# Kernel optimization log

Measured on AMD Instinct MI355X. Metric: run time of the kernel, lower is better.

Reference implementation:

```python
import jax, jax.numpy as jnp
import numpy as np

EPS = 1e-12          # sinkhorn_knopp epsilon
LOW, HIGH = 0.02, 0.98  # SquashedSigmoid bounds
N_ITERS = 10         # num_iterations
BATCH = 2097152


def setup_inputs() -> dict:
    key = jax.random.key(0)
    ks = jax.random.split(key, 9)
    dims = [6, 64, 32, 16, 9]
    inp = {"margins": jax.random.uniform(ks[0], (BATCH, 6), jnp.float32, 0.05, 1.0)}
    for i in range(4):
        fi, fo = dims[i], dims[i + 1]
        inp[f"W{i+1}"] = jax.random.normal(ks[1 + 2 * i], (fi, fo), jnp.float32) / np.float32(np.sqrt(fi))
        inp[f"b{i+1}"] = jnp.zeros((fo,), jnp.float32)
    return inp


def _mlp(x, W1, b1, W2, b2, W3, b3, W4, b4):
    h = jax.nn.relu(x @ W1 + b1)
    h = jax.nn.relu(h @ W2 + b2)
    h = jax.nn.relu(h @ W3 + b3)
    return h @ W4 + b4  # [B, 9]


def _tau(p4):
    # user-supplied tau: 4 positive params -> 3x3 matrix; 2x2 block padded with ones
    B = p4.shape[0]
    A = jnp.ones((B, 3, 3), p4.dtype)
    return A.at[:, :2, :2].set(p4.reshape(B, 2, 2))


def _sinkhorn_knopp(A, r, c):
    # batched row/col balancing; per-sample A is 3x3, r/c are length-3 margins
    for _ in range(N_ITERS):
        A = A * (r[:, :, None] / (A.sum(axis=2, keepdims=True) + EPS))
        A = A * (c[:, None, :] / (A.sum(axis=1, keepdims=True) + EPS))
    return A


def reference(margins, W1, b1, W2, b2, W3, b3, W4, b4):
    B = margins.shape[0]
    M, F = margins[:, 0:3], margins[:, 3:6]
    pars = _mlp(margins, W1, b1, W2, b2, W3, b3, W4, b4)
    muc = _tau(jnp.exp(pars[:, 0:4]))                     # [B,3,3]
    sqs = lambda x: LOW + (HIGH - LOW) * jax.nn.sigmoid(x)
    shm, shf = sqs(pars[:, 4:6]), sqs(pars[:, 6:8])
    V = jnp.exp(pars[:, -1])                              # [B]
    ones = jnp.ones((B, 1), margins.dtype)
    shm0 = jnp.concatenate([shm, ones], axis=1)           # [B,3]
    shf0 = jnp.concatenate([shf, ones], axis=1)
    mucm0, muc0f = M * shm0, F * shf0                     # row / col margins
    mum0, mu0f = M * (1 - shm0), F * (1 - shf0)
    muc = _sinkhorn_knopp(muc, mucm0, muc0f)              # [B,3,3]
    top = jnp.concatenate([muc, mum0[:, :, None]], axis=2)                    # [B,3,4]
    bot = jnp.concatenate([mu0f[:, None, :], jnp.zeros((B, 1, 1), margins.dtype)], axis=2)  # [B,1,4]
    mus = jnp.concatenate([top, bot], axis=1)             # [B,4,4]
    return (mus, V)
```

## Files before the change

kernel.cpp:

```cpp
#include <hip/hip_runtime.h>

typedef _Float16 f16x8 __attribute__((ext_vector_type(8)));
typedef _Float16 f16x4 __attribute__((ext_vector_type(4)));
typedef float    f32x4 __attribute__((ext_vector_type(4)));

static constexpr float kLOW  = 0.02f;
static constexpr float kHIGH = 0.98f;

__device__ __forceinline__ float fast_sigmoid(float v) {
    return 1.0f / (1.0f + __expf(-v));
}
__device__ __forceinline__ float fast_rcp(float v) {
    return __builtin_amdgcn_rcpf(v);
}

__global__ __launch_bounds__(256, 4) void sinkhorn_mlp_mfma(
    const float* __restrict__ margins,
    const float* __restrict__ W1, const float* __restrict__ b1,
    const float* __restrict__ W2, const float* __restrict__ b2,
    const float* __restrict__ W3, const float* __restrict__ b3,
    const float* __restrict__ W4, const float* __restrict__ b4,
    float* __restrict__ out_mus, float* __restrict__ out_V, int B)
{
    __shared__ __align__(16) char smem_all[4 * 9216];
    const int lane = threadIdx.x & 63;
    const int wid  = threadIdx.x >> 6;
    char* smem = smem_all + wid * 9216;

    const int n16 = lane & 15;
    const int q   = lane >> 4;

    const int row  = blockIdx.x * 256 + wid * 64 + lane;
    const int rowC = row < B ? row : (B - 1);

    float x[6];
    {
        const float* mp = margins + (size_t)rowC * 6;
#pragma unroll
        for (int i = 0; i < 6; ++i) x[i] = mp[i];
    }

    {
        f16x8 xr;
#pragma unroll
        for (int j = 0; j < 8; ++j) xr[j] = (_Float16)0.0f;
#pragma unroll
        for (int i = 0; i < 6; ++i) xr[i] = (_Float16)x[i];
        *(f16x8*)(smem + 8176 + lane * 16) = xr;
        if (lane == 0) {
            f16x8 z;
#pragma unroll
            for (int j = 0; j < 8; ++j) z[j] = (_Float16)0.0f;
            *(f16x8*)(smem + 9200) = z;
        }
    }

    f16x8 A1[4];
#pragma unroll
    for (int mt = 0; mt < 4; ++mt)
#pragma unroll
        for (int j = 0; j < 8; ++j) A1[mt][j] = (_Float16)0.0f;
    if (q == 0) {
#pragma unroll
        for (int mt = 0; mt < 4; ++mt)
#pragma unroll
            for (int j = 0; j < 6; ++j)
                A1[mt][j] = (_Float16)W1[j * 64 + mt * 16 + n16];
    }

    f16x8 A2w[2][2];
#pragma unroll
    for (int mt = 0; mt < 2; ++mt)
#pragma unroll
        for (int kt = 0; kt < 2; ++kt)
#pragma unroll
            for (int j = 0; j < 8; ++j)
                A2w[mt][kt][j] = (_Float16)W2[(kt*32 + q*8 + j)*32 + mt*16 + n16];

    f16x8 A3w;
#pragma unroll
    for (int j = 0; j < 8; ++j)
        A3w[j] = (_Float16)W3[(q*8 + j)*16 + n16];

    f32x4 b1v[4], b2v[2], b3v;
#pragma unroll
    for (int mt = 0; mt < 4; ++mt) b1v[mt] = *(const f32x4*)(b1 + mt*16 + q*4);
#pragma unroll
    for (int mt = 0; mt < 2; ++mt) b2v[mt] = *(const f32x4*)(b2 + mt*16 + q*4);
    b3v = *(const f32x4*)(b3 + q*4);

    f16x8 BX[4];
    {
        const int xo   = (q == 0) ? (8176 + n16 * 16) : 9200;
        const int step = (q == 0) ? 256 : 0;
#pragma unroll
        for (int nt = 0; nt < 4; ++nt)
            BX[nt] = *(const f16x8*)(smem + xo + nt * step);
    }
#pragma unroll
    for (int mt = 0; mt < 4; ++mt) {
#pragma unroll
        for (int nt = 0; nt < 4; ++nt) {
            f32x4 C = b1v[mt];
            C = __builtin_amdgcn_mfma_f32_16x16x32_f16(A1[mt], BX[nt], C, 0, 0, 0);
            f16x4 hv;
#pragma unroll
            for (int r = 0; r < 4; ++r) hv[r] = (_Float16)fmaxf(C[r], 0.0f);
            *(f16x4*)(smem + (nt*16 + n16) * 144 + mt*32 + q*8) = hv;
        }
    }

    f16x8 H1f[4][2];
#pragma unroll
    for (int nt = 0; nt < 4; ++nt)
#pragma unroll
        for (int kt = 0; kt < 2; ++kt)
            H1f[nt][kt] = *(const f16x8*)(smem + (nt*16 + n16) * 144 + kt*64 + q*16);
#pragma unroll
    for (int mt = 0; mt < 2; ++mt) {
#pragma unroll
        for (int nt = 0; nt < 4; ++nt) {
            f32x4 C = b2v[mt];
            C = __builtin_amdgcn_mfma_f32_16x16x32_f16(A2w[mt][0], H1f[nt][0], C, 0, 0, 0);
            C = __builtin_amdgcn_mfma_f32_16x16x32_f16(A2w[mt][1], H1f[nt][1], C, 0, 0, 0);
            f16x4 hv;
#pragma unroll
            for (int r = 0; r < 4; ++r) hv[r] = (_Float16)fmaxf(C[r], 0.0f);
            *(f16x4*)(smem + (nt*16 + n16) * 80 + mt*32 + q*8) = hv;
        }
    }

    f16x8 H2f[4];
#pragma unroll
    for (int nt = 0; nt < 4; ++nt)
        H2f[nt] = *(const f16x8*)(smem + (nt*16 + n16) * 80 + q*16);
#pragma unroll
    for (int nt = 0; nt < 4; ++nt) {
        f32x4 C = b3v;
        C = __builtin_amdgcn_mfma_f32_16x16x32_f16(A3w, H2f[nt], C, 0, 0, 0);
        f32x4 o;
#pragma unroll
        for (int r = 0; r < 4; ++r) o[r] = fmaxf(C[r], 0.0f);
        *(f32x4*)(smem + (nt*16 + n16) * 80 + q*16) = o;
    }

    float h3[16];
    {
        const char* rp = smem + lane * 80;
#pragma unroll
        for (int i = 0; i < 4; ++i)
            *(f32x4*)&h3[4*i] = *(const f32x4*)(rp + i * 16);
    }

    float p[9];
#pragma unroll
    for (int k = 0; k < 9; ++k) p[k] = fmaf(h3[0], W4[k], b4[k]);
#pragma unroll
    for (int j = 1; j < 16; ++j) {
        const float hj = h3[j];
        const float* w = W4 + j * 9;
#pragma unroll
        for (int k = 0; k < 9; ++k) p[k] = fmaf(hj, w[k], p[k]);
    }

    const float K00 = __expf(p[0]), K01 = __expf(p[1]);
    const float K10 = __expf(p[2]), K11 = __expf(p[3]);

    const float sh_m0 = kLOW + (kHIGH - kLOW) * fast_sigmoid(p[4]);
    const float sh_m1 = kLOW + (kHIGH - kLOW) * fast_sigmoid(p[5]);
    const float sh_f0 = kLOW + (kHIGH - kLOW) * fast_sigmoid(p[6]);
    const float sh_f1 = kLOW + (kHIGH - kLOW) * fast_sigmoid(p[7]);
    const float V = __expf(p[8]);

    const float M0 = x[0], M1 = x[1], M2 = x[2];
    const float F0 = x[3], F1 = x[4], F2 = x[5];

    const float r0 = M0 * sh_m0, r1 = M1 * sh_m1, r2 = M2;
    const float c0 = F0 * sh_f0, c1 = F1 * sh_f1, c2 = F2;
    const float mum0_0 = M0 * (1.0f - sh_m0), mum0_1 = M1 * (1.0f - sh_m1);
    const float mu0f_0 = F0 * (1.0f - sh_f0), mu0f_1 = F1 * (1.0f - sh_f1);

    const float rc2 = fast_rcp(c2);
    const float g0 = c0 * rc2, g1 = c1 * rc2;
    float v0 = 1.0f, v1 = 1.0f;
    float u0, u1, u2;
#pragma unroll
    for (int it = 0; it < 9; ++it) {
        const float s0 = fmaf(K00, v0, fmaf(K01, v1, 1.0f));
        const float s1 = fmaf(K10, v0, fmaf(K11, v1, 1.0f));
        const float s2 = v0 + v1 + 1.0f;
        u0 = r0 * fast_rcp(s0);
        u1 = r1 * fast_rcp(s1);
        u2 = r2 * fast_rcp(s2);
        const float t0 = fmaf(K00, u0, fmaf(K10, u1, u2));
        const float t1 = fmaf(K01, u0, fmaf(K11, u1, u2));
        const float t2 = u0 + u1 + u2;
        v0 = g0 * (t2 * fast_rcp(t0));
        v1 = g1 * (t2 * fast_rcp(t1));
    }
    float vf0, vf1, vf2;
    {
        const float s0 = fmaf(K00, v0, fmaf(K01, v1, 1.0f));
        const float s1 = fmaf(K10, v0, fmaf(K11, v1, 1.0f));
        const float s2 = v0 + v1 + 1.0f;
        u0 = r0 * fast_rcp(s0);
        u1 = r1 * fast_rcp(s1);
        u2 = r2 * fast_rcp(s2);
        const float t0 = fmaf(K00, u0, fmaf(K10, u1, u2));
        const float t1 = fmaf(K01, u0, fmaf(K11, u1, u2));
        const float t2 = u0 + u1 + u2;
        vf0 = c0 * fast_rcp(t0);
        vf1 = c1 * fast_rcp(t1);
        vf2 = c2 * fast_rcp(t2);
    }
    const float A00 = u0 * K00 * vf0, A01 = u0 * K01 * vf1, A02 = u0 * vf2;
    const float A10 = u1 * K10 * vf0, A11 = u1 * K11 * vf1, A12 = u1 * vf2;
    const float A20 = u2 * vf0,       A21 = u2 * vf1,       A22 = u2 * vf2;

    if (row < B) {
        float4* o = (float4*)(out_mus + (size_t)row * 16);
        o[0] = make_float4(A00, A01, A02, mum0_0);
        o[1] = make_float4(A10, A11, A12, mum0_1);
        o[2] = make_float4(A20, A21, A22, 0.0f);
        o[3] = make_float4(mu0f_0, mu0f_1, 0.0f, 0.0f);
        out_V[row] = V;
    }
}

extern "C" void kernel_launch(void* const* d_in, const int* in_sizes, int n_in,
                              void* d_out, int out_size, void* d_ws, size_t ws_size,
                              hipStream_t stream) {
    const float* margins = (const float*)d_in[0];
    const float* W1 = (const float*)d_in[1];
    const float* b1 = (const float*)d_in[2];
    const float* W2 = (const float*)d_in[3];
    const float* b2 = (const float*)d_in[4];
    const float* W3 = (const float*)d_in[5];
    const float* b3 = (const float*)d_in[6];
    const float* W4 = (const float*)d_in[7];
    const float* b4 = (const float*)d_in[8];

    const int B = in_sizes[0] / 6;
    float* out_mus = (float*)d_out;
    float* out_V   = out_mus + (size_t)B * 16;

    dim3 block(256);
    dim3 grid((B + 255) / 256);
    hipLaunchKernelGGL(sinkhorn_mlp_mfma, grid, block, 0, stream,
                       margins, W1, b1, W2, b2, W3, b3, W4, b4,
                       out_mus, out_V, B);
}
```

Before: 227.1 us.

## Precompute MFMA weight fragments in prep kernel and run last layer on MFMA

A one-block prep kernel converts the weights and biases into per-lane fp16 MFMA fragment layout in the workspace, so each main-kernel wave loads ready fragments with vector loads instead of strided scalar loads and fp32-to-fp16 conversions. The final 16-to-9 layer now runs as an MFMA with an fp16 layer-3 activation, replacing 144 scalar FMAs per row. Margins are read as float2 and the sigmoid uses the hardware reciprocal. This adds a second launch and lowers the last layer to fp16 inputs, which may affect accuracy.

Result: no change. 224.5 us (-1.2%).

```diff
diff --git a/kernel.cpp b/kernel.cpp
--- a/kernel.cpp
+++ b/kernel.cpp
@@ -7,19 +7,94 @@
 static constexpr float kLOW  = 0.02f;
 static constexpr float kHIGH = 0.98f;
 
-__device__ __forceinline__ float fast_sigmoid(float v) {
-    return 1.0f / (1.0f + __expf(-v));
-}
 __device__ __forceinline__ float fast_rcp(float v) {
     return __builtin_amdgcn_rcpf(v);
 }
-
-__global__ __launch_bounds__(256, 4) void sinkhorn_mlp_mfma(
-    const float* __restrict__ margins,
+__device__ __forceinline__ float fast_sigmoid(float v) {
+    return fast_rcp(1.0f + __expf(-v));
+}
+
+enum : int {
+    WS_A1 = 0,
+    WS_A2 = 4096,
+    WS_A3 = 8192,
+    WS_A4 = 9216,
+    WS_B1 = 10240,
+    WS_B2 = 14336,
+    WS_B3 = 16384,
+    WS_B4 = 17408,
+    WS_TOTAL = 18432
+};
+
+__global__ __launch_bounds__(256) void prep_frags(
     const float* __restrict__ W1, const float* __restrict__ b1,
     const float* __restrict__ W2, const float* __restrict__ b2,
     const float* __restrict__ W3, const float* __restrict__ b3,
     const float* __restrict__ W4, const float* __restrict__ b4,
+    char* __restrict__ ws)
+{
+    const int lane = threadIdx.x & 63;
+    const int wid  = threadIdx.x >> 6;
+    const int n16  = lane & 15;
+    const int q    = lane >> 4;
+
+    if (wid == 0) {
+#pragma unroll
+        for (int mt = 0; mt < 4; ++mt) {
+            f16x8 a;
+#pragma unroll
+            for (int j = 0; j < 8; ++j) a[j] = (_Float16)0.0f;
+            if (q == 0) {
+#pragma unroll
+                for (int j = 0; j < 6; ++j)
+                    a[j] = (_Float16)W1[j * 64 + mt * 16 + n16];
+            }
+            ((f16x8*)(ws + WS_A1))[mt * 64 + lane] = a;
+        }
+#pragma unroll
+        for (int mt = 0; mt < 4; ++mt)
+            ((f32x4*)(ws + WS_B1))[mt * 64 + lane] = *(const f32x4*)(b1 + mt * 16 + q * 4);
+    } else if (wid == 1) {
+#pragma unroll
+        for (int mt = 0; mt < 2; ++mt)
+#pragma unroll
+            for (int kt = 0; kt < 2; ++kt) {
+                f16x8 a;
+#pragma unroll
+                for (int j = 0; j < 8; ++j)
+                    a[j] = (_Float16)W2[(kt * 32 + q * 8 + j) * 32 + mt * 16 + n16];
+                ((f16x8*)(ws + WS_A2))[(mt * 2 + kt) * 64 + lane] = a;
+            }
+    } else if (wid == 2) {
+        f16x8 a3;
+#pragma unroll
+        for (int j = 0; j < 8; ++j)
+            a3[j] = (_Float16)W3[(q * 8 + j) * 16 + n16];
+        ((f16x8*)(ws + WS_A3))[lane] = a3;
+        f16x8 a4;
+#pragma unroll
+        for (int j = 0; j < 8; ++j) {
+            const int k = q * 8 + j;
+            a4[j] = (k < 16 && n16 < 9) ? (_Float16)W4[k * 9 + n16] : (_Float16)0.0f;
+        }
+        ((f16x8*)(ws + WS_A4))[lane] = a4;
+    } else {
+#pragma unroll
+        for (int mt = 0; mt < 2; ++mt)
+            ((f32x4*)(ws + WS_B2))[mt * 64 + lane] = *(const f32x4*)(b2 + mt * 16 + q * 4);
+        ((f32x4*)(ws + WS_B3))[lane] = *(const f32x4*)(b3 + q * 4);
+        f32x4 bb;
+#pragma unroll
+        for (int r = 0; r < 4; ++r) {
+            const int m = q * 4 + r;
+            bb[r] = (m < 9) ? b4[m] : 0.0f;
+        }
+        ((f32x4*)(ws + WS_B4))[lane] = bb;
+    }
+}
+
+__global__ __launch_bounds__(256, 4) void sinkhorn_mlp_mfma(
+    const float* __restrict__ margins, const char* __restrict__ ws,
     float* __restrict__ out_mus, float* __restrict__ out_V, int B)
 {
     __shared__ __align__(16) char smem_all[4 * 9216];
@@ -35,9 +110,9 @@
 
     float x[6];
     {
-        const float* mp = margins + (size_t)rowC * 6;
-#pragma unroll
-        for (int i = 0; i < 6; ++i) x[i] = mp[i];
+        const float2* mp = (const float2*)(margins + (size_t)rowC * 6);
+        const float2 a = mp[0], b = mp[1], c = mp[2];
+        x[0] = a.x; x[1] = a.y; x[2] = b.x; x[3] = b.y; x[4] = c.x; x[5] = c.y;
     }
 
     {
@@ -55,39 +130,24 @@
         }
     }
 
-    f16x8 A1[4];
-#pragma unroll
-    for (int mt = 0; mt < 4; ++mt)
-#pragma unroll
-        for (int j = 0; j < 8; ++j) A1[mt][j] = (_Float16)0.0f;
-    if (q == 0) {
-#pragma unroll
-        for (int mt = 0; mt < 4; ++mt)
-#pragma unroll
-            for (int j = 0; j < 6; ++j)
-                A1[mt][j] = (_Float16)W1[j * 64 + mt * 16 + n16];
-    }
-
-    f16x8 A2w[2][2];
+    f16x8 A1[4], A2w[2][2], A3w, A4w;
+#pragma unroll
+    for (int mt = 0; mt < 4; ++mt) A1[mt] = ((const f16x8*)(ws + WS_A1))[mt * 64 + lane];
 #pragma unroll
     for (int mt = 0; mt < 2; ++mt)
 #pragma unroll
         for (int kt = 0; kt < 2; ++kt)
-#pragma unroll
-            for (int j = 0; j < 8; ++j)
-                A2w[mt][kt][j] = (_Float16)W2[(kt*32 + q*8 + j)*32 + mt*16 + n16];
-
-    f16x8 A3w;
-#pragma unroll
-    for (int j = 0; j < 8; ++j)
-        A3w[j] = (_Float16)W3[(q*8 + j)*16 + n16];
-
-    f32x4 b1v[4], b2v[2], b3v;
-#pragma unroll
-    for (int mt = 0; mt < 4; ++mt) b1v[mt] = *(const f32x4*)(b1 + mt*16 + q*4);
-#pragma unroll
-    for (int mt = 0; mt < 2; ++mt) b2v[mt] = *(const f32x4*)(b2 + mt*16 + q*4);
-    b3v = *(const f32x4*)(b3 + q*4);
+            A2w[mt][kt] = ((const f16x8*)(ws + WS_A2))[(mt * 2 + kt) * 64 + lane];
+    A3w = ((const f16x8*)(ws + WS_A3))[lane];
+    A4w = ((const f16x8*)(ws + WS_A4))[lane];
+
+    f32x4 b1v[4], b2v[2], b3v, b4v;
+#pragma unroll
+    for (int mt = 0; mt < 4; ++mt) b1v[mt] = ((const f32x4*)(ws + WS_B1))[mt * 64 + lane];
+#pragma unroll
+    for (int mt = 0; mt < 2; ++mt) b2v[mt] = ((const f32x4*)(ws + WS_B2))[mt * 64 + lane];
+    b3v = ((const f32x4*)(ws + WS_B3))[lane];
+    b4v = ((const f32x4*)(ws + WS_B4))[lane];
 
     f16x8 BX[4];
     {
@@ -138,29 +198,31 @@
     for (int nt = 0; nt < 4; ++nt) {
         f32x4 C = b3v;
         C = __builtin_amdgcn_mfma_f32_16x16x32_f16(A3w, H2f[nt], C, 0, 0, 0);
-        f32x4 o;
-#pragma unroll
-        for (int r = 0; r < 4; ++r) o[r] = fmaxf(C[r], 0.0f);
-        *(f32x4*)(smem + (nt*16 + n16) * 80 + q*16) = o;
-    }
-
-    float h3[16];
-    {
-        const char* rp = smem + lane * 80;
-#pragma unroll
-        for (int i = 0; i < 4; ++i)
-            *(f32x4*)&h3[4*i] = *(const f32x4*)(rp + i * 16);
+        f16x4 hv;
+#pragma unroll
+        for (int r = 0; r < 4; ++r) hv[r] = (_Float16)fmaxf(C[r], 0.0f);
+        *(f16x4*)(smem + (nt*16 + n16) * 32 + q*8) = hv;
+    }
+
+    f16x8 B4[4];
+#pragma unroll
+    for (int nt = 0; nt < 4; ++nt) {
+        const int off = (q < 2) ? ((nt*16 + n16) * 32 + q * 16) : 9200;
+        B4[nt] = *(const f16x8*)(smem + off);
+    }
+#pragma unroll
+    for (int nt = 0; nt < 4; ++nt) {
+        f32x4 C = b4v;
+        C = __builtin_amdgcn_mfma_f32_16x16x32_f16(A4w, B4[nt], C, 0, 0, 0);
+        *(f32x4*)(smem + 2560 + (nt*16 + n16) * 80 + q * 16) = C;
     }
 
     float p[9];
-#pragma unroll
-    for (int k = 0; k < 9; ++k) p[k] = fmaf(h3[0], W4[k], b4[k]);
-#pragma unroll
-    for (int j = 1; j < 16; ++j) {
-        const float hj = h3[j];
-        const float* w = W4 + j * 9;
-#pragma unroll
-        for (int k = 0; k < 9; ++k) p[k] = fmaf(hj, w[k], p[k]);
+    {
+        const char* pr = smem + 2560 + lane * 80;
+        *(f32x4*)&p[0] = *(const f32x4*)(pr);
+        *(f32x4*)&p[4] = *(const f32x4*)(pr + 16);
+        p[8] = *(const float*)(pr + 32);
     }
 
     const float K00 = __expf(p[0]), K01 = __expf(p[1]);
@@ -243,10 +305,13 @@
     const int B = in_sizes[0] / 6;
     float* out_mus = (float*)d_out;
     float* out_V   = out_mus + (size_t)B * 16;
+    char*  ws      = (char*)d_ws;
+
+    hipLaunchKernelGGL(prep_frags, dim3(1), dim3(256), 0, stream,
+                       W1, b1, W2, b2, W3, b3, W4, b4, ws);
 
     dim3 block(256);
     dim3 grid((B + 255) / 256);
     hipLaunchKernelGGL(sinkhorn_mlp_mfma, grid, block, 0, stream,
-                       margins, W1, b1, W2, b2, W3, b3, W4, b4,
-                       out_mus, out_V, B);
-}
+                       margins, ws, out_mus, out_V, B);
+}
```
